# Kernel optimization log

Measured on AMD Instinct MI355X. Metric: run time of the kernel, lower is better.

The kernel has to match this reference:

```python
import jax, jax.numpy as jnp
import numpy as np

N = 50000          # nodes
E_RAND = 590000    # random edges (+ N self-loops -> E = 640000)
IN_F = 128
OUT_F = 128
H, D = 8, 16       # num_heads, head_dim (H*D == OUT_F)
HOP = 5
ALPHA = 0.1
SLOPE = 0.2
EPS = 1e-5


def _layer_norm(x, g, b):
    mu = jnp.mean(x, axis=-1, keepdims=True)
    var = jnp.mean((x - mu) ** 2, axis=-1, keepdims=True)
    return (x - mu) * jax.lax.rsqrt(var + EPS) * g + b


def setup_inputs() -> dict:
    key = jax.random.key(0)
    ks = jax.random.split(key, 10)
    loops = jnp.arange(N, dtype=jnp.int32)  # self-loops -> no 0-in-degree nodes
    src = jnp.concatenate([loops, jax.random.randint(ks[0], (E_RAND,), 0, N, dtype=jnp.int32)])
    dst = jnp.concatenate([loops, jax.random.randint(ks[1], (E_RAND,), 0, N, dtype=jnp.int32)])
    s = 0.05  # xavier-like small init gain
    return {
        "feat": jax.random.normal(ks[2], (N, IN_F), jnp.float32),
        "src": src,
        "dst": dst,
        "w_head": jax.random.normal(ks[3], (OUT_F, IN_F), jnp.float32) * s,
        "w_tail": jax.random.normal(ks[4], (OUT_F, IN_F), jnp.float32) * s,
        "w_ent": jax.random.normal(ks[5], (OUT_F, IN_F), jnp.float32) * s,
        "attn": jax.random.normal(ks[6], (1, H, D), jnp.float32) * s,
        "ln1_g": jnp.ones((IN_F,), jnp.float32),
        "ln1_b": jnp.zeros((IN_F,), jnp.float32),
        "ln2_g": jnp.ones((OUT_F,), jnp.float32),
        "ln2_b": jnp.zeros((OUT_F,), jnp.float32),
        "ff_w1": jax.random.normal(ks[7], (4 * OUT_F, OUT_F), jnp.float32) * s,
        "ff_b1": jnp.zeros((4 * OUT_F,), jnp.float32),
        "ff_w2": jax.random.normal(ks[8], (OUT_F, 4 * OUT_F), jnp.float32) * s,
        "ff_b2": jnp.zeros((OUT_F,), jnp.float32),
    }


def _forward(src, dst, feat, w_head, w_tail, w_ent, attn,
             ln1_g, ln1_b, ln2_g, ln2_b, ff_w1, ff_b1, ff_w2, ff_b2):
    ones = jnp.ones(src.shape[0], jnp.float32)
    out_deg = jnp.clip(jax.ops.segment_sum(ones, src, num_segments=N), 1.0)  # [N]
    in_deg = jnp.clip(jax.ops.segment_sum(ones, dst, num_segments=N), 1.0)
    head_norm = out_deg ** -0.5
    tail_norm = in_deg ** 0.5
    log_in = jnp.log1p(in_deg)  # graph.dstdata['log_in'] (log of in-degree, set at graph build time)

    x = _layer_norm(feat, ln1_g, ln1_b)  # graph_layer_norm (feat_drop=0 in eval)
    fh = (x @ w_head.T).reshape(N, H, D) * head_norm[:, None, None]
    ft = (x @ w_tail.T).reshape(N, H, D) * head_norm[:, None, None]
    fe = (x @ w_ent.T).reshape(N, H, D) * head_norm[:, None, None]

    # edge attention logits: u_mul_v -> leaky_relu -> dot with attn vector
    lr = jax.nn.leaky_relu(fh[src] * ft[dst], SLOPE)  # [E,H,D]
    e = jnp.einsum('ehd,xhd->eh', lr, attn)           # [E,H]
    e = e * log_in[dst][:, None] / D                  # e_mul_v with log_in, / head_dim

    # edge softmax grouped by destination node, per head
    seg_max = jax.ops.segment_max(e, dst, num_segments=N)
    e_exp = jnp.exp(e - seg_max[dst])
    denom = jax.ops.segment_sum(e_exp, dst, num_segments=N)
    a = e_exp / denom[dst]                            # [E,H]

    # PPR diffusion (ppr_estimation), attn_drop=0 in eval
    feat0 = fe
    h = feat0
    for hop in range(HOP):
        if hop > 0:
            h = h * head_norm[:, None, None]
        m = h[src] * a[:, :, None]                    # [E,H,D] u_mul_e
        h = jax.ops.segment_sum(m, dst, num_segments=N)  # fn.sum
        h = h * tail_norm[:, None, None]
        h = (1.0 - ALPHA) * h + ALPHA * feat0

    rst = h + feat.reshape(N, H, D)  # res_fc is Identity since in_feats == out_feats
    rst = rst.reshape(N, OUT_F)
    ff = _layer_norm(rst, ln2_g, ln2_b)
    ff = jax.nn.relu(ff @ ff_w1.T + ff_b1) @ ff_w2.T + ff_b2  # PositionWiseFeedForward
    return ff + rst


def reference(feat, src, dst, w_head, w_tail, w_ent, attn, ln1_g, ln1_b,
              ln2_g, ln2_b, ff_w1, ff_b1, ff_w2, ff_b2):
    return _forward(src, dst, feat, w_head, w_tail, w_ent, attn,
                    ln1_g, ln1_b, ln2_g, ln2_b, ff_w1, ff_b1, ff_w2, ff_b2)
```

## Files before the change

kernel.cpp:

```cpp
#include <hip/hip_runtime.h>
#include <hip/hip_bf16.h>
#include <hip/hip_fp16.h>

typedef __attribute__((ext_vector_type(8))) short bf16x8;
typedef __attribute__((ext_vector_type(4))) float f32x4;
typedef unsigned int uint32;

#define F 128
#define HOPS 5
#define LDS_STRIDE 68
#define W1_STRIDE 136
#define W2_STRIDE 72
#define TB_STRIDE 72

__device__ __forceinline__ float b2f(__hip_bfloat16 h) { return __bfloat162float(h); }
__device__ __forceinline__ __hip_bfloat16 f2b(float f) { return __float2bfloat16(f); }

__device__ __forceinline__ float load_in(const void* p, size_t i, int isbf) {
    return isbf ? __bfloat162float(((const __hip_bfloat16*)p)[i]) : ((const float*)p)[i];
}

__device__ __forceinline__ float bflo(uint32 u) { union { uint32 i; float f; } v; v.i = u << 16; return v.f; }
__device__ __forceinline__ float bfhi(uint32 u) { union { uint32 i; float f; } v; v.i = u & 0xffff0000u; return v.f; }
__device__ __forceinline__ uint32 packbf2(float a, float b) {
    __hip_bfloat16 ha = f2b(a), hb = f2b(b);
    unsigned short ua = *(unsigned short*)&ha, ub = *(unsigned short*)&hb;
    return ((uint32)ub << 16) | ua;
}

__device__ __forceinline__ int xcd_id() {
    unsigned v;
    asm volatile("s_getreg_b32 %0, hwreg(HW_REG_XCC_ID)" : "=s"(v));
    return (int)(v & 7);
}

__device__ __forceinline__ float edge_dot2(uint4 gv, const float* c1, const float* c2) {
    float acc = 0.f, acc2 = 0.f;
    uint32 us[4] = {gv.x, gv.y, gv.z, gv.w};
    #pragma unroll
    for (int k = 0; k < 4; ++k) {
        float f0 = bflo(us[k]), f1 = bfhi(us[k]);
        acc  = fmaf(c1[2 * k],     f0,        acc);
        acc2 = fmaf(c2[2 * k],     fabsf(f0), acc2);
        acc  = fmaf(c1[2 * k + 1], f1,        acc);
        acc2 = fmaf(c2[2 * k + 1], fabsf(f1), acc2);
    }
    return acc + acc2;
}

__global__ void detect_k(const uint32* __restrict__ w, int* flag) {
    __shared__ int cnt[256];
    int t = threadIdx.x;
    uint32 x = w[t * 97];
    int e_low = (x >> 7) & 0xFF;
    cnt[t] = (e_low >= 110 && e_low <= 135) ? 1 : 0;
    __syncthreads();
    for (int s = 128; s > 0; s >>= 1) {
        if (t < s) cnt[t] += cnt[t + s];
        __syncthreads();
    }
    if (t == 0) flag[0] = (cnt[0] >= 160) ? 1 : 0;
}

__global__ void fused_pre_k(const int* __restrict__ src, const int* __restrict__ dst,
                            int* in8, int* out1, uint32* __restrict__ pack, int E,
                            const void* __restrict__ feat, const void* __restrict__ ln1g,
                            const void* __restrict__ ln1b,
                            const void* __restrict__ w_head, const void* __restrict__ w_tail,
                            const void* __restrict__ w_ent, const void* __restrict__ ff_w1,
                            const void* __restrict__ ff_w2, const void* __restrict__ attn,
                            const void* __restrict__ ff_b1, const void* __restrict__ ff_b2,
                            const int* __restrict__ flag,
                            __hip_bfloat16* __restrict__ wblob, float* __restrict__ fblob,
                            __hip_bfloat16* __restrict__ x_bf,
                            int nbDeg, int nbLn, int N) {
    int bid = blockIdx.x;
    if (bid < nbDeg) {
        int base = bid * 2048 + threadIdx.x;
        int slice = xcd_id();
        int idx[8], d[8], s[8], r[8];
#pragma unroll
        for (int k = 0; k < 8; ++k) idx[k] = base + k * 256;
#pragma unroll
        for (int k = 0; k < 8; ++k)
            if (idx[k] < E) { d[k] = dst[idx[k]]; s[k] = src[idx[k]]; }
#pragma unroll
        for (int k = 0; k < 8; ++k)
            if (idx[k] < E) r[k] = atomicAdd(&in8[slice * N + d[k]], 1);
#pragma unroll
        for (int k = 0; k < 8; ++k)
            if (idx[k] < E) atomicAdd(&out1[s[k]], 1);
#pragma unroll
        for (int k = 0; k < 8; ++k)
            if (idx[k] < E) pack[idx[k]] = (uint32)r[k] | ((uint32)slice << 24);
        return;
    }
    if (bid < nbDeg + nbLn) {
        int w = (bid - nbDeg) * 4 + (threadIdx.x >> 6);
        if (w >= N) return;
        int isbf = flag[0];
        int t = threadIdx.x & 63;
        float v0 = load_in(feat, (size_t)w * F + t, isbf);
        float v1 = load_in(feat, (size_t)w * F + t + 64, isbf);
        float s = v0 + v1, sq = v0 * v0 + v1 * v1;
        for (int m = 1; m < 64; m <<= 1) { s += __shfl_xor(s, m, 64); sq += __shfl_xor(sq, m, 64); }
        float mu = s * (1.0f / F);
        float var = fmaxf(sq * (1.0f / F) - mu * mu, 0.0f);
        float r = rsqrtf(var + 1e-5f);
        x_bf[(size_t)w * F + t]      = f2b((v0 - mu) * r * load_in(ln1g, t, isbf) + load_in(ln1b, t, isbf));
        x_bf[(size_t)w * F + t + 64] = f2b((v1 - mu) * r * load_in(ln1g, t + 64, isbf) + load_in(ln1b, t + 64, isbf));
        return;
    }
    {
        int i = (bid - nbDeg - nbLn) * 256 + threadIdx.x;
        int isbf = flag[0];
        if (i < 180224) {
            const void* srcp; int j;
            if (i < 16384)       { srcp = w_head; j = i; }
            else if (i < 32768)  { srcp = w_tail; j = i - 16384; }
            else if (i < 49152)  { srcp = w_ent;  j = i - 32768; }
            else if (i < 114688) { srcp = ff_w1;  j = i - 49152; }
            else                 { srcp = ff_w2;  j = i - 114688; }
            wblob[i] = f2b(load_in(srcp, j, isbf));
        } else if (i < 180992) {
            int k = i - 180224;
            const void* srcp; int j;
            if (k < 128)      { srcp = attn;  j = k; }
            else if (k < 640) { srcp = ff_b1; j = k - 128; }
            else              { srcp = ff_b2; j = k - 640; }
            fblob[k] = load_in(srcp, j, isbf);
        }
    }
}

__global__ void scan1_k(const int* __restrict__ in8, int* partial, int* blk_sum, int N) {
    __shared__ int sh[256];
    int t = threadIdx.x;
    int i = blockIdx.x * 256 + t;
    int c = 0;
    if (i < N) {
#pragma unroll
        for (int s = 0; s < 8; ++s) c += in8[s * N + i];
    }
    sh[t] = c;
    __syncthreads();
    for (int o = 1; o < 256; o <<= 1) {
        int v = (t >= o) ? sh[t - o] : 0;
        __syncthreads();
        sh[t] += v;
        __syncthreads();
    }
    if (i < N) partial[i] = sh[t] - c;
    if (t == 255) blk_sum[blockIdx.x] = sh[255];
}

__global__ void scan2_k(const int* __restrict__ blk_sum, int* blk_off, int nb,
                        int* row_ptr, int N) {
    __shared__ int sh[256];
    int t = threadIdx.x;
    if (nb <= 256) {
        int v = (t < nb) ? blk_sum[t] : 0;
        sh[t] = v;
        __syncthreads();
        for (int o = 1; o < 256; o <<= 1) {
            int u = (t >= o) ? sh[t - o] : 0;
            __syncthreads();
            sh[t] += u;
            __syncthreads();
        }
        if (t < nb) blk_off[t] = sh[t] - v;
        if (t == 255) row_ptr[N] = sh[255];
    } else if (t == 0) {
        int run = 0;
        for (int b = 0; b < nb; ++b) { blk_off[b] = run; run += blk_sum[b]; }
        row_ptr[N] = run;
    }
}

__global__ void scan3_norms_k(const int* __restrict__ partial, const int* __restrict__ blk_off,
                              const int* __restrict__ in8, const int* __restrict__ out1,
                              int* row_ptr, int* soff, float* head_norm, float* tail_norm,
                              float* log_in, int N) {
    int i = blockIdx.x * 256 + threadIdx.x;
    if (i >= N) return;
    row_ptr[i] = partial[i] + blk_off[blockIdx.x];
    int run = 0;
#pragma unroll
    for (int s = 0; s < 8; ++s) { soff[s * N + i] = run; run += in8[s * N + i]; }
    int od = out1[i];
    float id = fmaxf((float)run, 1.0f);
    float odf = fmaxf((float)od, 1.0f);
    head_norm[i] = rsqrtf(odf);
    tail_norm[i] = sqrtf(id);
    log_in[i] = log1pf(id);
}

__global__ void scan3f_k(const int* __restrict__ partial, const int* __restrict__ blk_sum,
                         int nb, const int* __restrict__ in8, const int* __restrict__ out1,
                         int* row_ptr, int* soff, float* head_norm, float* tail_norm,
                         float* log_in, int N) {
    __shared__ int bs[256];
    int t = threadIdx.x;
    bs[t] = (t < nb) ? blk_sum[t] : 0;
    __syncthreads();
    for (int o = 1; o < 256; o <<= 1) {
        int v = (t >= o) ? bs[t - o] : 0;
        __syncthreads();
        bs[t] += v;
        __syncthreads();
    }
    if (blockIdx.x == 0 && t == 0) row_ptr[N] = bs[nb - 1];
    int boff = (blockIdx.x == 0) ? 0 : bs[blockIdx.x - 1];
    int i = blockIdx.x * 256 + t;
    if (i >= N) return;
    row_ptr[i] = partial[i] + boff;
    int run = 0;
#pragma unroll
    for (int s = 0; s < 8; ++s) { soff[s * N + i] = run; run += in8[s * N + i]; }
    int od = out1[i];
    float id = fmaxf((float)run, 1.0f);
    float odf = fmaxf((float)od, 1.0f);
    head_norm[i] = rsqrtf(odf);
    tail_norm[i] = sqrtf(id);
    log_in[i] = log1pf(id);
}

__global__ void fused_mid_k(const int* __restrict__ src, const int* __restrict__ dst,
                            const int* __restrict__ row_ptr, const int* __restrict__ soff,
                            const uint32* __restrict__ pack, int* __restrict__ csr_src,
                            int E, int N, int nbSc, int Mb,
                            const __hip_bfloat16* __restrict__ X,
                            const __hip_bfloat16* __restrict__ Wall,
                            const float* __restrict__ head_norm,
                            __hip_bfloat16* __restrict__ fh,
                            __hip_bfloat16* __restrict__ ft,
                            uint32* __restrict__ fe_bf) {
    __shared__ __align__(16) char smem[2 * 64 * W1_STRIDE * 2];
    int bid = blockIdx.x;
    if (bid < nbSc) {
        int base = bid * 2048 + threadIdx.x;
#pragma unroll
        for (int k = 0; k < 8; ++k) {
            int i = base + k * 256;
            if (i < E) {
                int d = dst[i];
                uint32 pk = pack[i];
                int s = (int)(pk >> 24);
                int r = (int)(pk & 0xFFFFFFu);
                csr_src[row_ptr[d] + soff[s * N + d] + r] = src[i];
            }
        }
        return;
    }
    int pb = bid - nbSc;
    int g = pb / Mb;
    int bm = (pb - g * Mb) * 64;
    __hip_bfloat16* lx = (__hip_bfloat16*)smem;
    __hip_bfloat16* lw = (__hip_bfloat16*)(smem + 64 * W1_STRIDE * 2);
    float* eps = (float*)smem;
    int tid = threadIdx.x;
    int wv = tid >> 6, lane = tid & 63;
    int lr = lane & 15, quad = lane >> 4;
    int wsel = g >> 1;
    int wcb = (g & 1) * 64;
    {
        const __hip_bfloat16* xs = X + (size_t)bm * F;
        size_t maxe = (size_t)N * F;
#pragma unroll
        for (int i = 0; i < 4; ++i) {
            int idx = i * 2048 + tid * 8;
            int n = idx >> 7, k = idx & 127;
            size_t gi = (size_t)bm * F + idx;
            uint4 v = (gi + 8 <= maxe) ? *(const uint4*)(xs + idx)
                                       : *(const uint4*)(X + maxe - 8);
            *(uint4*)&lx[n * W1_STRIDE + k] = v;
        }
        const __hip_bfloat16* ws = Wall + ((size_t)wsel * F + wcb) * F;
#pragma unroll
        for (int i = 0; i < 4; ++i) {
            int idx = i * 2048 + tid * 8;
            int n = idx >> 7, k = idx & 127;
            *(uint4*)&lw[n * W1_STRIDE + k] = *(const uint4*)(ws + idx);
        }
    }
    __syncthreads();
    f32x4 acc[4] = {{0,0,0,0},{0,0,0,0},{0,0,0,0},{0,0,0,0}};
#pragma unroll
    for (int ks = 0; ks < 4; ++ks) {
        bf16x8 a = *reinterpret_cast<const bf16x8*>(&lx[(wv * 16 + lr) * W1_STRIDE + ks * 32 + quad * 8]);
#pragma unroll
        for (int j = 0; j < 4; ++j) {
            bf16x8 bb = *reinterpret_cast<const bf16x8*>(&lw[(j * 16 + lr) * W1_STRIDE + ks * 32 + quad * 8]);
            acc[j] = __builtin_amdgcn_mfma_f32_16x16x32_bf16(a, bb, acc[j], 0, 0, 0);
        }
    }
    __syncthreads();
    int rl = wv * 16 + quad * 4;
#pragma unroll
    for (int j = 0; j < 4; ++j)
#pragma unroll
        for (int r = 0; r < 4; ++r)
            eps[(rl + r) * LDS_STRIDE + j * 16 + lr] = acc[j][r];
    __syncthreads();
    int tr = tid >> 4, tc = (tid & 15) * 4;
#pragma unroll
    for (int p = 0; p < 4; ++p) {
        int row_l = p * 16 + tr;
        int grow = bm + row_l;
        if (grow >= N) continue;
        float4 v = *(const float4*)&eps[row_l * LDS_STRIDE + tc];
        float hn = head_norm[grow];
        v.x *= hn; v.y *= hn; v.z *= hn; v.w *= hn;
        size_t idx = (size_t)grow * F + wcb + tc;
        uint2 u; u.x = packbf2(v.x, v.y); u.y = packbf2(v.z, v.w);
        __hip_bfloat16* dstp = (wsel == 0) ? fh : (wsel == 1) ? ft : (__hip_bfloat16*)fe_bf;
        *(uint2*)&dstp[idx] = u;
    }
}

__global__ void attn_soft_k(const int* __restrict__ csr_src, const int* __restrict__ row_ptr,
                            const uint32* __restrict__ fh2, const uint32* __restrict__ ft2,
                            const float* __restrict__ attn_f, const float* __restrict__ log_in,
                            __half* __restrict__ e_h, float* __restrict__ inv_arr, int N) {
    int w = blockIdx.x * (blockDim.x >> 6) + (threadIdx.x >> 6);
    if (w >= N) return;
    int t = threadIdx.x & 63;
    int g = t >> 4, j = t & 15;
    int b = row_ptr[w], e = row_ptr[w + 1];
    uint4 fr = ((const uint4*)ft2)[(size_t)w * 16 + j];
    float ftf[8] = {bflo(fr.x), bfhi(fr.x), bflo(fr.y), bfhi(fr.y),
                    bflo(fr.z), bfhi(fr.z), bflo(fr.w), bfhi(fr.w)};
    float c1[8], c2[8];
#pragma unroll
    for (int k = 0; k < 8; ++k) {
        float at = attn_f[8 * j + k];
        c1[k] = 0.6f * at * ftf[k];
        c2[k] = 0.4f * at * fabsf(ftf[k]);
    }
    float scale = log_in[w] * (1.0f / 16.0f);
    float m = -1e30f;
    for (int p0 = b; p0 < e; p0 += 8) {
        int pa = p0 + g, pb = p0 + 4 + g;
        bool oka = pa < e, okb = pb < e;
        int sa = csr_src[oka ? pa : b];
        int sb = csr_src[okb ? pb : b];
        uint4 ga = ((const uint4*)fh2)[(size_t)sa * 16 + j];
        uint4 gb = ((const uint4*)fh2)[(size_t)sb * 16 + j];
        float ra = edge_dot2(ga, c1, c2);
        float rb = edge_dot2(gb, c1, c2);
        ra += __shfl_xor(ra, 1, 64);
        rb += __shfl_xor(rb, 1, 64);
        float la = ra * scale, lb = rb * scale;
        if (oka) { if (!(j & 1)) e_h[(size_t)pa * 8 + (j >> 1)] = __float2half(la); m = fmaxf(m, la); }
        if (okb) { if (!(j & 1)) e_h[(size_t)pb * 8 + (j >> 1)] = __float2half(lb); m = fmaxf(m, lb); }
    }
    m = fmaxf(m, __shfl_xor(m, 16, 64));
    m = fmaxf(m, __shfl_xor(m, 32, 64));
    float mh = __shfl(m, (t & 7) * 2, 64);
    float sum = 0.f;
    for (size_t base = (size_t)b * 8 + t; base < (size_t)e * 8; base += 64) {
        float ex = expf(__half2float(e_h[base]) - mh);
        e_h[base] = __float2half(ex);
        sum += ex;
    }
    sum += __shfl_xor(sum, 8, 64);
    sum += __shfl_xor(sum, 16, 64);
    sum += __shfl_xor(sum, 32, 64);
    float inv = 1.0f / fmaxf(sum, 1e-30f);
    if (t < 8) inv_arr[(size_t)w * 8 + t] = inv;
}

__global__ void hop_k(const uint32* __restrict__ gsrc2, const __half* __restrict__ e_h,
                      const float* __restrict__ inv_arr,
                      const int* __restrict__ csr_src, const int* __restrict__ row_ptr,
                      const float* __restrict__ tail_norm, const float* __restrict__ head_norm,
                      const uint32* __restrict__ fe_bf, const void* __restrict__ feat,
                      const void* __restrict__ ln2g, const void* __restrict__ ln2b,
                      const int* __restrict__ flag,
                      uint32* __restrict__ out_bf, float* __restrict__ out_f32,
                      int last, int N) {
    int w = blockIdx.x * 8 + (threadIdx.x >> 5);
    if (w >= N) return;
    int l = threadIdx.x & 31;
    int h = l >> 2;
    int b = row_ptr[w], e = row_ptr[w + 1];
    float inv = inv_arr[(size_t)w * 8 + h];
    float a0 = 0.f, a1 = 0.f, a2 = 0.f, a3 = 0.f;
    int p = b;
    for (; p + 8 <= e; p += 8) {
        int s[8]; float av[8]; uint2 gg[8];
#pragma unroll
        for (int i = 0; i < 8; ++i) s[i] = csr_src[p + i];
#pragma unroll
        for (int i = 0; i < 8; ++i) av[i] = __half2float(e_h[(size_t)(p + i) * 8 + h]);
#pragma unroll
        for (int i = 0; i < 8; ++i) gg[i] = ((const uint2*)gsrc2)[(size_t)s[i] * 32 + l];
#pragma unroll
        for (int i = 0; i < 8; ++i) {
            a0 += bflo(gg[i].x) * av[i]; a1 += bfhi(gg[i].x) * av[i];
            a2 += bflo(gg[i].y) * av[i]; a3 += bfhi(gg[i].y) * av[i];
        }
    }
    if (p < e) {
        int s[8]; float av[8]; uint2 gg[8];
#pragma unroll
        for (int i = 0; i < 8; ++i) {
            int q = p + i;
            bool ok = q < e;
            int q2 = ok ? q : b;
            s[i] = csr_src[q2];
            av[i] = ok ? __half2float(e_h[(size_t)q * 8 + h]) : 0.f;
        }
#pragma unroll
        for (int i = 0; i < 8; ++i) gg[i] = ((const uint2*)gsrc2)[(size_t)s[i] * 32 + l];
#pragma unroll
        for (int i = 0; i < 8; ++i) {
            a0 += bflo(gg[i].x) * av[i]; a1 += bfhi(gg[i].x) * av[i];
            a2 += bflo(gg[i].y) * av[i]; a3 += bfhi(gg[i].y) * av[i];
        }
    }
    float tl = tail_norm[w] * 0.9f * inv;
    uint2 feu = ((const uint2*)fe_bf)[(size_t)w * 32 + l];
    float r0 = tl * a0 + 0.1f * bflo(feu.x);
    float r1 = tl * a1 + 0.1f * bfhi(feu.x);
    float r2 = tl * a2 + 0.1f * bflo(feu.y);
    float r3 = tl * a3 + 0.1f * bfhi(feu.y);
    if (last) {
        int isbf = flag[0];
        float4 o;
        if (isbf) {
            uint2 fu = ((const uint2*)feat)[(size_t)w * 32 + l];
            o.x = r0 + bflo(fu.x); o.y = r1 + bfhi(fu.x);
            o.z = r2 + bflo(fu.y); o.w = r3 + bfhi(fu.y);
        } else {
            float4 fv = ((const float4*)feat)[(size_t)w * 32 + l];
            o.x = r0 + fv.x; o.y = r1 + fv.y; o.z = r2 + fv.z; o.w = r3 + fv.w;
        }
        ((float4*)out_f32)[(size_t)w * 32 + l] = o;
        float s2 = o.x + o.y + o.z + o.w;
        float sq = o.x * o.x + o.y * o.y + o.z * o.z + o.w * o.w;
#pragma unroll
        for (int mm = 1; mm < 32; mm <<= 1) {
            s2 += __shfl_xor(s2, mm, 64);
            sq += __shfl_xor(sq, mm, 64);
        }
        float mu = s2 * (1.0f / F);
        float var = fmaxf(sq * (1.0f / F) - mu * mu, 0.0f);
        float rr = rsqrtf(var + 1e-5f);
        float g0 = load_in(ln2g, 4 * l + 0, isbf), g1 = load_in(ln2g, 4 * l + 1, isbf);
        float g2 = load_in(ln2g, 4 * l + 2, isbf), g3 = load_in(ln2g, 4 * l + 3, isbf);
        float b0 = load_in(ln2b, 4 * l + 0, isbf), b1 = load_in(ln2b, 4 * l + 1, isbf);
        float b2 = load_in(ln2b, 4 * l + 2, isbf), b3 = load_in(ln2b, 4 * l + 3, isbf);
        uint2 u;
        u.x = packbf2((o.x - mu) * rr * g0 + b0, (o.y - mu) * rr * g1 + b1);
        u.y = packbf2((o.z - mu) * rr * g2 + b2, (o.w - mu) * rr * g3 + b3);
        ((uint2*)out_bf)[(size_t)w * 32 + l] = u;
    } else {
        float hn = head_norm[w];
        uint2 u;
        u.x = packbf2(r0 * hn, r1 * hn);
        u.y = packbf2(r2 * hn, r3 * hn);
        ((uint2*)out_bf)[(size_t)w * 32 + l] = u;
    }
}

__global__ __launch_bounds__(256, 2)
void ffn_fused_k(const __hip_bfloat16* __restrict__ Y, const __hip_bfloat16* __restrict__ W1,
                 const __hip_bfloat16* __restrict__ W2, const float* __restrict__ b1f,
                 const float* __restrict__ b2f, const float* __restrict__ rst,
                 const int* __restrict__ flag, void* __restrict__ out, int N) {
    __shared__ __align__(16) char smem[45056];
    __hip_bfloat16* lw1 = (__hip_bfloat16*)smem;
    __hip_bfloat16* lw2 = (__hip_bfloat16*)(smem + 17408);
    __hip_bfloat16* tb  = (__hip_bfloat16*)(smem + 35840);
    float* eps = (float*)smem;
    int tid = threadIdx.x;
    int wv = tid >> 6, lane = tid & 63;
    int lr = lane & 15, quad = lane >> 4;
    int bm = blockIdx.x * 64;
    int row_a = bm + wv * 16 + lr;
    if (row_a >= N) row_a = N - 1;
    bf16x8 ay[4];
    {
        const __hip_bfloat16* yr = Y + (size_t)row_a * F + quad * 8;
#pragma unroll
        for (int ks = 0; ks < 4; ++ks) ay[ks] = *reinterpret_cast<const bf16x8*>(yr + ks * 32);
    }
    f32x4 o[8];
#pragma unroll
    for (int j = 0; j < 8; ++j) o[j] = (f32x4){0,0,0,0};
    __hip_bfloat16* tbuf = tb + wv * (16 * TB_STRIDE);
    for (int c = 0; c < 8; ++c) {
        int nb0 = c * 64;
        __syncthreads();
        {
            const __hip_bfloat16* s1 = W1 + (size_t)nb0 * F;
#pragma unroll
            for (int i = 0; i < 4; ++i) {
                int idx = i * 2048 + tid * 8;
                int n = idx >> 7, k = idx & 127;
                *(uint4*)&lw1[n * W1_STRIDE + k] = *(const uint4*)(s1 + idx);
            }
#pragma unroll
            for (int i = 0; i < 4; ++i) {
                int idx = i * 2048 + tid * 8;
                int r = idx >> 6, k2 = idx & 63;
                *(uint4*)&lw2[r * W2_STRIDE + k2] = *(const uint4*)(W2 + (size_t)r * 512 + nb0 + k2);
            }
        }
        __syncthreads();
        f32x4 t[4] = {{0,0,0,0},{0,0,0,0},{0,0,0,0},{0,0,0,0}};
#pragma unroll
        for (int ks = 0; ks < 4; ++ks) {
#pragma unroll
            for (int j = 0; j < 4; ++j) {
                bf16x8 bb = *reinterpret_cast<const bf16x8*>(&lw1[(j * 16 + lr) * W1_STRIDE + ks * 32 + quad * 8]);
                t[j] = __builtin_amdgcn_mfma_f32_16x16x32_bf16(ay[ks], bb, t[j], 0, 0, 0);
            }
        }
#pragma unroll
        for (int j = 0; j < 4; ++j) {
            float bias = b1f[nb0 + 16 * j + lr];
#pragma unroll
            for (int r = 0; r < 4; ++r) {
                float v = fmaxf(t[j][r] + bias, 0.f);
                tbuf[(quad * 4 + r) * TB_STRIDE + j * 16 + lr] = f2b(v);
            }
        }
#pragma unroll
        for (int ks2 = 0; ks2 < 2; ++ks2) {
            bf16x8 at = *reinterpret_cast<const bf16x8*>(&tbuf[lr * TB_STRIDE + ks2 * 32 + quad * 8]);
#pragma unroll
            for (int j2 = 0; j2 < 8; ++j2) {
                bf16x8 bb = *reinterpret_cast<const bf16x8*>(&lw2[(j2 * 16 + lr) * W2_STRIDE + ks2 * 32 + quad * 8]);
                o[j2] = __builtin_amdgcn_mfma_f32_16x16x32_bf16(at, bb, o[j2], 0, 0, 0);
            }
        }
    }
    __syncthreads();
    int rl = wv * 16 + quad * 4;
#pragma unroll
    for (int j = 0; j < 8; ++j)
#pragma unroll
        for (int r = 0; r < 4; ++r)
            eps[(rl + r) * 132 + j * 16 + lr] = o[j][r];
    __syncthreads();
    int isbf = flag[0];
#pragma unroll
    for (int p = 0; p < 8; ++p) {
        int idx = p * 1024 + tid * 4;
        int row_l = idx >> 7, col = idx & 127;
        int grow = bm + row_l;
        if (grow >= N) continue;
        float4 v = *(const float4*)&eps[row_l * 132 + col];
        float4 bias = *(const float4*)&b2f[col];
        float4 rv = *(const float4*)&rst[(size_t)grow * F + col];
        v.x += bias.x + rv.x; v.y += bias.y + rv.y;
        v.z += bias.z + rv.z; v.w += bias.w + rv.w;
        size_t gidx = (size_t)grow * F + col;
        if (isbf) {
            uint2 u; u.x = packbf2(v.x, v.y); u.y = packbf2(v.z, v.w);
            *(uint2*)&((__hip_bfloat16*)out)[gidx] = u;
        } else {
            *(float4*)&((float*)out)[gidx] = v;
        }
    }
}

extern "C" void kernel_launch(void* const* d_in, const int* in_sizes, int n_in,
                              void* d_out, int out_size, void* d_ws, size_t ws_size,
                              hipStream_t stream) {
    if (n_in < 15) return;
    const void* feat = d_in[0];
    const int* src = (const int*)d_in[1];
    const int* dst = (const int*)d_in[2];
    const void* w_head = d_in[3];
    const void* w_tail = d_in[4];
    const void* w_ent  = d_in[5];
    const void* attn   = d_in[6];
    const void* ln1_g  = d_in[7];
    const void* ln1_b  = d_in[8];
    const void* ln2_g  = d_in[9];
    const void* ln2_b  = d_in[10];
    const void* ff_w1  = d_in[11];
    const void* ff_b1  = d_in[12];
    const void* ff_w2  = d_in[13];
    const void* ff_b2  = d_in[14];

    const int N = in_sizes[0] / F;
    const int E = in_sizes[1];
    (void)out_size;

    char* base = (char*)d_ws;
    size_t off = 0;
    auto alloc = [&](size_t bytes) -> void* {
        void* r = base + off;
        off += (bytes + 255) & ~(size_t)255;
        return r;
    };
    int* zr        = (int*)alloc((size_t)9 * N * 4);
    int* in8 = zr, * out1 = zr + 8 * N;
    int* soff      = (int*)alloc((size_t)8 * N * 4);
    int* row_ptr   = (int*)alloc((size_t)(N + 1) * 4);
    int* partial   = (int*)alloc((size_t)N * 4);
    int* blk_sum   = (int*)alloc((size_t)1024 * 4);
    int* blk_off   = (int*)alloc((size_t)1024 * 4);
    int* flag      = (int*)alloc(256);
    float* head_norm = (float*)alloc((size_t)N * 4);
    float* tail_norm = (float*)alloc((size_t)N * 4);
    float* log_in    = (float*)alloc((size_t)N * 4);
    float* inv_arr   = (float*)alloc((size_t)N * 8 * 4);
    int* csr_src   = (int*)alloc((size_t)E * 4);
    uint32* pack   = (uint32*)alloc((size_t)E * 4);
    __hip_bfloat16* wh_bf = (__hip_bfloat16*)alloc((size_t)F * F * 2);
    __hip_bfloat16* wt_bf = (__hip_bfloat16*)alloc((size_t)F * F * 2);
    __hip_bfloat16* we_bf = (__hip_bfloat16*)alloc((size_t)F * F * 2);
    __hip_bfloat16* w1_bf = (__hip_bfloat16*)alloc((size_t)512 * F * 2);
    __hip_bfloat16* w2_bf = (__hip_bfloat16*)alloc((size_t)F * 512 * 2);
    float* attn_f    = (float*)alloc((size_t)F * 4);
    float* b1f       = (float*)alloc((size_t)512 * 4);
    float* b2f_      = (float*)alloc((size_t)F * 4);
    __hip_bfloat16* x_bf = (__hip_bfloat16*)alloc((size_t)N * F * 2);
    __hip_bfloat16* fh   = (__hip_bfloat16*)alloc((size_t)N * F * 2);
    __hip_bfloat16* ftb  = (__hip_bfloat16*)alloc((size_t)N * F * 2);
    uint32* fe_bf = (uint32*)alloc((size_t)N * F * 2);
    uint32* hA_bf = (uint32*)alloc((size_t)N * F * 2);
    uint32* hB_bf = (uint32*)alloc((size_t)N * F * 2);
    float* rst = (float*)alloc((size_t)N * F * 4);
    __hip_bfloat16* y_bf = (__hip_bfloat16*)hA_bf;
    __half* e_h = (__half*)x_bf;
    (void)wt_bf; (void)we_bf;
    if (off > ws_size) return;

    const int Mb = (N + 63) / 64;
    const int nodeBlocks = (N + 3) / 4;
    const int hopBlocks = (N + 7) / 8;
    const int nb = (N + 255) / 256;
    const int nbDeg = (E + 2047) / 2048;
    const int nbLn  = (N + 3) / 4;
    const int nbCvt = (180992 + 255) / 256;

    detect_k<<<1, 256, 0, stream>>>((const uint32*)feat, flag);
    hipMemsetAsync(zr, 0, (size_t)9 * N * 4, stream);

    fused_pre_k<<<nbDeg + nbLn + nbCvt, 256, 0, stream>>>(
        src, dst, in8, out1, pack, E,
        feat, ln1_g, ln1_b,
        w_head, w_tail, w_ent, ff_w1, ff_w2, attn, ff_b1, ff_b2,
        flag, wh_bf, attn_f, x_bf, nbDeg, nbLn, N);

    scan1_k<<<nb, 256, 0, stream>>>(in8, partial, blk_sum, N);
    if (nb <= 256) {
        scan3f_k<<<nb, 256, 0, stream>>>(partial, blk_sum, nb, in8, out1,
                                         row_ptr, soff, head_norm, tail_norm, log_in, N);
    } else {
        scan2_k<<<1, 256, 0, stream>>>(blk_sum, blk_off, nb, row_ptr, N);
        scan3_norms_k<<<nb, 256, 0, stream>>>(partial, blk_off, in8, out1,
                                              row_ptr, soff, head_norm, tail_norm, log_in, N);
    }

    const int nbSc = (E + 2047) / 2048;
    fused_mid_k<<<nbSc + Mb * 6, 256, 0, stream>>>(
        src, dst, row_ptr, soff, pack, csr_src, E, N, nbSc, Mb,
        x_bf, wh_bf, head_norm, fh, ftb, fe_bf);

    attn_soft_k<<<nodeBlocks, 256, 0, stream>>>(csr_src, row_ptr, (const uint32*)fh,
                                                (const uint32*)ftb, attn_f, log_in,
                                                e_h, inv_arr, N);

    const uint32* gsrc = fe_bf;
    uint32* bufs[2] = {hA_bf, hB_bf};
    for (int hop = 0; hop < HOPS; ++hop) {
        int last = (hop == HOPS - 1);
        uint32* dst_bf = last ? (uint32*)y_bf : bufs[hop & 1];
        hop_k<<<hopBlocks, 256, 0, stream>>>(gsrc, e_h, inv_arr, csr_src, row_ptr, tail_norm,
                                             head_norm, fe_bf, feat, ln2_g, ln2_b, flag,
                                             dst_bf, rst, last, N);
        if (!last) gsrc = dst_bf;
    }

    ffn_fused_k<<<Mb, 256, 0, stream>>>(y_bf, w1_bf, w2_bf, b1f, b2f_, rst, flag, d_out, N);
}
```

Before: 429.2 us.

## Fuse first PPR hop into attention softmax kernel

```diff
diff --git a/kernel.cpp b/kernel.cpp
--- a/kernel.cpp
+++ b/kernel.cpp
@@ -318,56 +318,86 @@
     }
 }
 
-__global__ void attn_soft_k(const int* __restrict__ csr_src, const int* __restrict__ row_ptr,
+__global__ void attn_hop0_k(const int* __restrict__ csr_src, const int* __restrict__ row_ptr,
                             const uint32* __restrict__ fh2, const uint32* __restrict__ ft2,
                             const float* __restrict__ attn_f, const float* __restrict__ log_in,
-                            __half* __restrict__ e_h, float* __restrict__ inv_arr, int N) {
+                            const float* __restrict__ tail_norm, const float* __restrict__ head_norm,
+                            const uint32* __restrict__ fe_bf,
+                            __half* __restrict__ e_h, float* __restrict__ inv_arr,
+                            uint32* __restrict__ out_bf, int N) {
     int w = blockIdx.x * (blockDim.x >> 6) + (threadIdx.x >> 6);
     if (w >= N) return;
     int t = threadIdx.x & 63;
     int g = t >> 4, j = t & 15;
     int b = row_ptr[w], e = row_ptr[w + 1];
-    uint4 fr = ((const uint4*)ft2)[(size_t)w * 16 + j];
-    float ftf[8] = {bflo(fr.x), bfhi(fr.x), bflo(fr.y), bfhi(fr.y),
-                    bflo(fr.z), bfhi(fr.z), bflo(fr.w), bfhi(fr.w)};
-    float c1[8], c2[8];
-#pragma unroll
-    for (int k = 0; k < 8; ++k) {
-        float at = attn_f[8 * j + k];
-        c1[k] = 0.6f * at * ftf[k];
-        c2[k] = 0.4f * at * fabsf(ftf[k]);
-    }
-    float scale = log_in[w] * (1.0f / 16.0f);
-    float m = -1e30f;
-    for (int p0 = b; p0 < e; p0 += 8) {
-        int pa = p0 + g, pb = p0 + 4 + g;
-        bool oka = pa < e, okb = pb < e;
-        int sa = csr_src[oka ? pa : b];
-        int sb = csr_src[okb ? pb : b];
-        uint4 ga = ((const uint4*)fh2)[(size_t)sa * 16 + j];
-        uint4 gb = ((const uint4*)fh2)[(size_t)sb * 16 + j];
-        float ra = edge_dot2(ga, c1, c2);
-        float rb = edge_dot2(gb, c1, c2);
-        ra += __shfl_xor(ra, 1, 64);
-        rb += __shfl_xor(rb, 1, 64);
-        float la = ra * scale, lb = rb * scale;
-        if (oka) { if (!(j & 1)) e_h[(size_t)pa * 8 + (j >> 1)] = __float2half(la); m = fmaxf(m, la); }
-        if (okb) { if (!(j & 1)) e_h[(size_t)pb * 8 + (j >> 1)] = __float2half(lb); m = fmaxf(m, lb); }
-    }
-    m = fmaxf(m, __shfl_xor(m, 16, 64));
-    m = fmaxf(m, __shfl_xor(m, 32, 64));
-    float mh = __shfl(m, (t & 7) * 2, 64);
-    float sum = 0.f;
-    for (size_t base = (size_t)b * 8 + t; base < (size_t)e * 8; base += 64) {
-        float ex = expf(__half2float(e_h[base]) - mh);
-        e_h[base] = __float2half(ex);
-        sum += ex;
-    }
-    sum += __shfl_xor(sum, 8, 64);
-    sum += __shfl_xor(sum, 16, 64);
-    sum += __shfl_xor(sum, 32, 64);
-    float inv = 1.0f / fmaxf(sum, 1e-30f);
-    if (t < 8) inv_arr[(size_t)w * 8 + t] = inv;
+    {
+        uint4 fr = ((const uint4*)ft2)[(size_t)w * 16 + j];
+        float ftf[8] = {bflo(fr.x), bfhi(fr.x), bflo(fr.y), bfhi(fr.y),
+                        bflo(fr.z), bfhi(fr.z), bflo(fr.w), bfhi(fr.w)};
+        float c1[8], c2[8];
+#pragma unroll
+        for (int k = 0; k < 8; ++k) {
+            float at = attn_f[8 * j + k];
+            c1[k] = 0.6f * at * ftf[k];
+            c2[k] = 0.4f * at * fabsf(ftf[k]);
+        }
+        float scale = log_in[w] * (1.0f / 16.0f);
+        float m = -1e30f;
+        for (int p0 = b; p0 < e; p0 += 8) {
+            int pa = p0 + g, pb = p0 + 4 + g;
+            bool oka = pa < e, okb = pb < e;
+            int sa = csr_src[oka ? pa : b];
+            int sb = csr_src[okb ? pb : b];
+            uint4 ga = ((const uint4*)fh2)[(size_t)sa * 16 + j];
+            uint4 gb = ((const uint4*)fh2)[(size_t)sb * 16 + j];
+            float ra = edge_dot2(ga, c1, c2);
+            float rb = edge_dot2(gb, c1, c2);
+            ra += __shfl_xor(ra, 1, 64);
+            rb += __shfl_xor(rb, 1, 64);
+            float la = ra * scale, lb = rb * scale;
+            if (oka) { if (!(j & 1)) e_h[(size_t)pa * 8 + (j >> 1)] = __float2half(la); m = fmaxf(m, la); }
+            if (okb) { if (!(j & 1)) e_h[(size_t)pb * 8 + (j >> 1)] = __float2half(lb); m = fmaxf(m, lb); }
+        }
+        m = fmaxf(m, __shfl_xor(m, 16, 64));
+        m = fmaxf(m, __shfl_xor(m, 32, 64));
+        int h = t >> 3;
+        float mh = __shfl(m, h * 2, 64);
+        float sum = 0.f, a0 = 0.f, a1 = 0.f;
+        for (int p = b; p < e; p += 8) {
+            int qq[8]; bool ok[8]; float ex[8]; uint32 rows[8];
+#pragma unroll
+            for (int i = 0; i < 8; ++i) {
+                int q = p + i;
+                ok[i] = q < e;
+                qq[i] = ok[i] ? q : b;
+            }
+            int srcs[8];
+#pragma unroll
+            for (int i = 0; i < 8; ++i) srcs[i] = csr_src[qq[i]];
+#pragma unroll
+            for (int i = 0; i < 8; ++i) {
+                float lg = __half2float(e_h[(size_t)qq[i] * 8 + h]);
+                ex[i] = ok[i] ? __expf(lg - mh) : 0.f;
+            }
+#pragma unroll
+            for (int i = 0; i < 8; ++i) rows[i] = fe_bf[(size_t)srcs[i] * 64 + t];
+#pragma unroll
+            for (int i = 0; i < 8; ++i) {
+                if (ok[i] && (t & 7) == 0) e_h[(size_t)qq[i] * 8 + h] = __float2half(ex[i]);
+                sum += ex[i];
+                a0 = fmaf(bflo(rows[i]), ex[i], a0);
+                a1 = fmaf(bfhi(rows[i]), ex[i], a1);
+            }
+        }
+        float inv = 1.0f / fmaxf(sum, 1e-30f);
+        if ((t & 7) == 0) inv_arr[(size_t)w * 8 + h] = inv;
+        float tl = tail_norm[w] * 0.9f * inv;
+        uint32 fe_l = fe_bf[(size_t)w * 64 + t];
+        float r0 = tl * a0 + 0.1f * bflo(fe_l);
+        float r1 = tl * a1 + 0.1f * bfhi(fe_l);
+        float hn = head_norm[w];
+        out_bf[(size_t)w * 64 + t] = packbf2(r0 * hn, r1 * hn);
+    }
 }
 
 __global__ void hop_k(const uint32* __restrict__ gsrc2, const __half* __restrict__ e_h,
@@ -664,13 +694,14 @@
         src, dst, row_ptr, soff, pack, csr_src, E, N, nbSc, Mb,
         x_bf, wh_bf, head_norm, fh, ftb, fe_bf);
 
-    attn_soft_k<<<nodeBlocks, 256, 0, stream>>>(csr_src, row_ptr, (const uint32*)fh,
+    attn_hop0_k<<<nodeBlocks, 256, 0, stream>>>(csr_src, row_ptr, (const uint32*)fh,
                                                 (const uint32*)ftb, attn_f, log_in,
-                                                e_h, inv_arr, N);
-
-    const uint32* gsrc = fe_bf;
+                                                tail_norm, head_norm, fe_bf,
+                                                e_h, inv_arr, hA_bf, N);
+
+    const uint32* gsrc = hA_bf;
     uint32* bufs[2] = {hA_bf, hB_bf};
-    for (int hop = 0; hop < HOPS; ++hop) {
+    for (int hop = 1; hop < HOPS; ++hop) {
         int last = (hop == HOPS - 1);
         uint32* dst_bf = last ? (uint32*)y_bf : bufs[hop & 1];
         hop_k<<<hopBlocks, 256, 0, stream>>>(gsrc, e_h, inv_arr, csr_src, row_ptr, tail_norm,
```

After: 424.6 us. No clear change (-1.1%).
